# Optimization experiments

Hardware: AMD Instinct MI355X
Metric: run time of the kernel (lower is better)

Reference implementation:

```python
import jax, jax.numpy as jnp
import numpy as np

EPS = 1e-7  # K.epsilon()
SIZE_IN, IN_CAPS, KSIZE, STRIDE, CAPS, ROUTINGS = 14, 32, 3, 2, 32, 3
SIZE_OUT = (SIZE_IN - KSIZE) // STRIDE + 1  # 6
P = SIZE_OUT * SIZE_OUT          # 36 parent positions
C = KSIZE * KSIZE * IN_CAPS      # 288 child capsules per parent


def _child_parent_map():
    idx = []
    valid = range(0, SIZE_IN - KSIZE + 1, STRIDE)
    for row in valid:
        for col in valid:
            for kr in range(KSIZE):
                start = (row + kr) * SIZE_IN + col
                idx.extend(range(start, start + KSIZE))
    return np.asarray(idx, dtype=np.int32).reshape(P, KSIZE * KSIZE)

CPM = _child_parent_map()  # [P, K^2] static gather indices


def _em_routing(in_act, votes, beta_a, beta_v):
    # in_act: [B,P,C,1,1]; votes: [B,P,C,O,16]
    O = CAPS
    rr = jnp.full(votes.shape[:4] + (1,), 1.0 / O, dtype=votes.dtype)
    bv = beta_v.reshape(1, 1, 1, O, 1)
    ba = beta_a.reshape(1, 1, 1, O)
    out_act = means = None
    for i in range(ROUTINGS):
        lambd = 0.01 * (1.0 - 0.95 ** i)
        # ---- M step ----
        rr_scaled = rr * in_act                                   # [B,P,C,O,1]
        rr_sum = jnp.sum(rr_scaled, axis=2, keepdims=True)        # [B,P,1,O,1]
        means = jnp.sum(rr_scaled * votes, axis=2, keepdims=True) / (rr_sum + EPS)  # [B,P,1,O,16]
        std = jnp.sqrt(jnp.sum(rr_scaled * jnp.square(votes - means), axis=2, keepdims=True) / (rr_sum + EPS))
        costs = bv + jnp.log(std + EPS) * rr_sum                  # [B,P,1,O,16]
        out_act = jax.nn.sigmoid(lambd * (ba - jnp.sum(costs, axis=-1)))[..., None]  # [B,P,1,O,1]
        # ---- E step ----
        if i < ROUTINGS - 1:
            prob_exp = -jnp.sum(jnp.square(votes - means) / (2.0 * jnp.square(std) + EPS), axis=-1, keepdims=True)
            prob_main = -jnp.sum(jnp.log(std + EPS), axis=-1, keepdims=True)
            zz = jnp.log(out_act + EPS) + prob_main + prob_exp   # [B,P,C,O,1]
            rr = jax.nn.softmax(zz, axis=3)
    return out_act, means


def setup_inputs() -> dict:
    key = jax.random.key(0)
    k1, k2, k3, k4, k5 = jax.random.split(key, 5)
    B = 8
    return {
        "in_act": jax.random.uniform(k1, (B, SIZE_IN, SIZE_IN, IN_CAPS, 1), dtype=jnp.float32),
        "in_pose": jax.random.normal(k2, (B, SIZE_IN, SIZE_IN, IN_CAPS, 4, 4), dtype=jnp.float32),
        "W": jax.random.normal(k3, (1, 1, C, CAPS, 4, 4), dtype=jnp.float32) * 0.1,
        "beta_a": jax.random.normal(k4, (CAPS,), dtype=jnp.float32),
        "beta_v": jax.random.normal(k5, (CAPS,), dtype=jnp.float32),
    }


def reference(in_act, in_pose, W, beta_a, beta_v):
    B = in_act.shape[0]
    act = in_act.reshape(B, SIZE_IN * SIZE_IN, IN_CAPS)
    pose = in_pose.reshape(B, SIZE_IN * SIZE_IN, IN_CAPS, 4, 4)
    # gather children for each parent window -> [B,P,C,...]
    act_g = act[:, CPM].reshape(B, P, C, 1, 1)
    pose_g = pose[:, CPM].reshape(B, P, C, 4, 4)
    # votes[b,p,c,o,i,j] = sum_k pose_g[b,p,c,i,k] * W[c,o,k,j]
    votes = jnp.einsum('bpcik,cokj->bpcoij', pose_g, W.reshape(C, CAPS, 4, 4))
    votes = votes.reshape(B, P, C, CAPS, 16)
    out_act, out_pose = _em_routing(act_g, votes, beta_a, beta_v)
    out_act = out_act.reshape(B, SIZE_OUT, SIZE_OUT, CAPS, 1)
    out_pose = out_pose.reshape(B, SIZE_OUT, SIZE_OUT, CAPS, 4, 4)
    return out_act, out_pose
```

## Files before the change

kernel.cpp:

```cpp
#include <hip/hip_runtime.h>
#include <math.h>

#define EPS 1e-7f

constexpr int SIZE_IN = 14;
constexpr int P_  = 36;
constexpr int Cc  = 288;
constexpr int O_  = 32;
constexpr int THREADS = 256;

struct __align__(16) SMem {
    float pose[Cc * 16];
    float act[Cc];
    float red[4][O_][33];
    float mean[O_][17];
    float iv[O_][17];
    float zb[O_];
};

#define F4_TO_ARR(dst, off, f4) \
    dst[(off)+0] = (f4).x; dst[(off)+1] = (f4).y; dst[(off)+2] = (f4).z; dst[(off)+3] = (f4).w;

template<int CTRL>
__device__ __forceinline__ float dppf(float x) {
    int xi = __builtin_bit_cast(int, x);
    return __builtin_bit_cast(float,
        __builtin_amdgcn_update_dpp(xi, xi, CTRL, 0xf, 0xf, true));
}
__device__ __forceinline__ float swz16(float x) {
    return __builtin_bit_cast(float,
        __builtin_amdgcn_ds_swizzle(__builtin_bit_cast(int, x), 0x401F));
}
__device__ __forceinline__ float red32_max(float x) {
    x = fmaxf(x, dppf<0xB1>(x));
    x = fmaxf(x, dppf<0x4E>(x));
    x = fmaxf(x, dppf<0x141>(x));
    x = fmaxf(x, dppf<0x140>(x));
    x = fmaxf(x, swz16(x));
    return x;
}
__device__ __forceinline__ float red32_sum(float x) {
    x += dppf<0xB1>(x);
    x += dppf<0x4E>(x);
    x += dppf<0x141>(x);
    x += dppf<0x140>(x);
    x += swz16(x);
    return x;
}
__device__ __forceinline__ float red16_sum(float x) {
    x += dppf<0xB1>(x);
    x += dppf<0x4E>(x);
    x += dppf<0x141>(x);
    x += dppf<0x140>(x);
    return x;
}

template<bool HASE, bool LAST>
__device__ __forceinline__ void em_pass(
    SMem& sm, const float* __restrict__ W,
    const float* __restrict__ beta_a, const float* __restrict__ beta_v,
    float lambda, int bp, float* __restrict__ out)
{
    const int tid = threadIdx.x;
    const int o  = tid & 31;
    const int ci = tid >> 5;

    float m[16], iv[16], zb = 0.f;
    if (HASE) {
        #pragma unroll
        for (int j = 0; j < 16; ++j) { m[j] = sm.mean[o][j]; iv[j] = sm.iv[o][j]; }
        zb = sm.zb[o];
    }

    float S0 = 0.f, S1[16], S2[16];
    #pragma unroll
    for (int j = 0; j < 16; ++j) { S1[j] = 0.f; S2[j] = 0.f; }

    const float4* wp0 = reinterpret_cast<const float4*>(W + (size_t)(ci * O_ + o) * 16);
    float4 nw0 = wp0[0], nw1 = wp0[1], nw2 = wp0[2], nw3 = wp0[3];
    const float4* pp0 = reinterpret_cast<const float4*>(&sm.pose[ci * 16]);
    float4 np0 = pp0[0], np1 = pp0[1], np2 = pp0[2], np3 = pp0[3];

    #pragma unroll 2
    for (int t = 0; t < 36; ++t) {
        const int c = t * 8 + ci;
        float w[16], q[16];
        F4_TO_ARR(w, 0, nw0) F4_TO_ARR(w, 4, nw1) F4_TO_ARR(w, 8, nw2) F4_TO_ARR(w, 12, nw3)
        F4_TO_ARR(q, 0, np0) F4_TO_ARR(q, 4, np1) F4_TO_ARR(q, 8, np2) F4_TO_ARR(q, 12, np3)
        if (t + 1 < 36) {
            const int cn = c + 8;
            const float4* wn = reinterpret_cast<const float4*>(W + (size_t)(cn * O_ + o) * 16);
            nw0 = wn[0]; nw1 = wn[1]; nw2 = wn[2]; nw3 = wn[3];
            const float4* pn = reinterpret_cast<const float4*>(&sm.pose[cn * 16]);
            np0 = pn[0]; np1 = pn[1]; np2 = pn[2]; np3 = pn[3];
        }

        float v[16];
        #pragma unroll
        for (int i = 0; i < 4; ++i) {
            #pragma unroll
            for (int jj = 0; jj < 4; ++jj) {
                float acc = q[i*4+0] * w[0*4+jj];
                acc = fmaf(q[i*4+1], w[1*4+jj], acc);
                acc = fmaf(q[i*4+2], w[2*4+jj], acc);
                acc = fmaf(q[i*4+3], w[3*4+jj], acc);
                v[i*4+jj] = acc;
            }
        }

        float ws;
        if (HASE) {
            float s = 0.f;
            #pragma unroll
            for (int j = 0; j < 16; ++j) { float d = v[j] - m[j]; s = fmaf(d * d, iv[j], s); }
            float zz = zb - s;
            float mx = red32_max(zz);
            float e = __expf(zz - mx);
            float sum = red32_sum(e);
            float rr = e / sum;
            ws = rr * sm.act[c];
        } else {
            ws = sm.act[c] * (1.0f / 32.0f);
        }

        S0 += ws;
        #pragma unroll
        for (int j = 0; j < 16; ++j) {
            float t0 = ws * v[j];
            S1[j] += t0;
            S2[j] = fmaf(t0, v[j], S2[j]);
        }
    }

    S0 += __shfl_xor(S0, 32);
    #pragma unroll
    for (int j = 0; j < 16; ++j) {
        S1[j] += __shfl_xor(S1[j], 32);
        S2[j] += __shfl_xor(S2[j], 32);
    }
    if (!(tid & 32)) {
        const int wv = tid >> 6;
        float* r = sm.red[wv][o];
        r[0] = S0;
        #pragma unroll
        for (int j = 0; j < 16; ++j) { r[1 + j] = S1[j]; r[17 + j] = S2[j]; }
    }
    __syncthreads();

    #pragma unroll
    for (int half = 0; half < 2; ++half) {
        const int of = (tid >> 4) + half * 16, jf = tid & 15;
        const float* r0 = sm.red[0][of];
        const float* r1 = sm.red[1][of];
        const float* r2 = sm.red[2][of];
        const float* r3 = sm.red[3][of];
        float s0 = r0[0] + r1[0] + r2[0] + r3[0];
        float s1 = r0[1+jf] + r1[1+jf] + r2[1+jf] + r3[1+jf];
        float s2 = r0[17+jf] + r1[17+jf] + r2[17+jf] + r3[17+jf];
        float denom = s0 + EPS;
        float mj = s1 / denom;
        float varn = fmaxf(s2 - 2.f * mj * s1 + mj * mj * s0, 0.f);
        float sd = sqrtf(varn / denom);
        float sumlog = red16_sum(__logf(sd + EPS));
        if (!LAST) {
            sm.mean[of][jf] = mj;
            sm.iv[of][jf] = 1.f / fmaf(2.f * sd, sd, EPS);
            if (jf == 0) {
                float cost = fmaf(16.f, beta_v[of], s0 * sumlog);
                float oact = 1.f / (1.f + __expf(-(lambda * (beta_a[of] - cost))));
                sm.zb[of] = __logf(oact + EPS) - sumlog;
            }
        } else {
            out[8 * P_ * O_ + (size_t)(bp * O_ + of) * 16 + jf] = mj;
            if (jf == 0) {
                float cost = fmaf(16.f, beta_v[of], s0 * sumlog);
                float oact = 1.f / (1.f + __expf(-(lambda * (beta_a[of] - cost))));
                out[bp * O_ + of] = oact;
            }
        }
    }
    __syncthreads();
}

__global__ __launch_bounds__(THREADS, 2) void convcaps_kernel(
    const float* __restrict__ in_act, const float* __restrict__ in_pose,
    const float* __restrict__ W, const float* __restrict__ beta_a,
    const float* __restrict__ beta_v, float* __restrict__ out)
{
    __shared__ SMem sm;
    const int bp = blockIdx.x;
    const int b  = bp / P_;
    const int p  = bp % P_;
    const int tid = threadIdx.x;
    const int row0 = (p / 6) * 2, col0 = (p % 6) * 2;

    for (int f = tid; f < 9 * 128; f += THREADS) {
        const int qw = f >> 7, r = f & 127;
        const int pix = (row0 + qw / 3) * SIZE_IN + (col0 + qw % 3);
        reinterpret_cast<float4*>(sm.pose)[qw * 128 + r] =
            reinterpret_cast<const float4*>(in_pose + (size_t)(b * 196 + pix) * 512)[r];
    }
    for (int idx = tid; idx < Cc; idx += THREADS) {
        const int qw = idx >> 5, ic = idx & 31;
        const int pix = (row0 + qw / 3) * SIZE_IN + (col0 + qw % 3);
        sm.act[idx] = in_act[(size_t)(b * 196 + pix) * 32 + ic];
    }
    __syncthreads();

    em_pass<false, false>(sm, W, beta_a, beta_v, 0.0f,      bp, out);
    em_pass<true,  false>(sm, W, beta_a, beta_v, 0.0005f,   bp, out);
    em_pass<true,  true >(sm, W, beta_a, beta_v, 0.000975f, bp, out);
}

extern "C" void kernel_launch(void* const* d_in, const int* in_sizes, int n_in,
                              void* d_out, int out_size, void* d_ws, size_t ws_size,
                              hipStream_t stream) {
    const float* in_act  = (const float*)d_in[0];
    const float* in_pose = (const float*)d_in[1];
    const float* W       = (const float*)d_in[2];
    const float* beta_a  = (const float*)d_in[3];
    const float* beta_v  = (const float*)d_in[4];
    float* out = (float*)d_out;

    convcaps_kernel<<<dim3(8 * P_), dim3(THREADS), 0, stream>>>(
        in_act, in_pose, W, beta_a, beta_v, out);
}
```

Before: 143.8 us.

## Split child capsules across four blocks per parent with multi-kernel routing passes

Each routing iteration becomes its own kernel launch, and each parent position's 288 children are split across 4 blocks. Partial sufficient statistics go to a workspace buffer and are reduced by the next pass or by a final output kernel. The grid grows from 288 to 1152 blocks, which is meant to fill the GPU's compute units better. The cost is three extra launches, global round-trips for the partial sums, and pose/act reloaded in every pass. The old fused kernel is kept as a fallback when the workspace is too small.

```diff
diff --git a/kernel.cpp b/kernel.cpp
--- a/kernel.cpp
+++ b/kernel.cpp
@@ -7,7 +7,233 @@
 constexpr int P_  = 36;
 constexpr int Cc  = 288;
 constexpr int O_  = 32;
+constexpr int G_  = 4;
+constexpr int CG  = Cc / G_;
+constexpr int NTG = CG / 8;
 constexpr int THREADS = 256;
+constexpr int NBP = 8 * P_;
+
+template<int CTRL>
+__device__ __forceinline__ float dppf(float x) {
+    int xi = __builtin_bit_cast(int, x);
+    return __builtin_bit_cast(float,
+        __builtin_amdgcn_update_dpp(xi, xi, CTRL, 0xf, 0xf, true));
+}
+__device__ __forceinline__ float swz16(float x) {
+    return __builtin_bit_cast(float,
+        __builtin_amdgcn_ds_swizzle(__builtin_bit_cast(int, x), 0x401F));
+}
+__device__ __forceinline__ float red32_max(float x) {
+    x = fmaxf(x, dppf<0xB1>(x));
+    x = fmaxf(x, dppf<0x4E>(x));
+    x = fmaxf(x, dppf<0x141>(x));
+    x = fmaxf(x, dppf<0x140>(x));
+    x = fmaxf(x, swz16(x));
+    return x;
+}
+__device__ __forceinline__ float red32_sum(float x) {
+    x += dppf<0xB1>(x);
+    x += dppf<0x4E>(x);
+    x += dppf<0x141>(x);
+    x += dppf<0x140>(x);
+    x += swz16(x);
+    return x;
+}
+__device__ __forceinline__ float red16_sum(float x) {
+    x += dppf<0xB1>(x);
+    x += dppf<0x4E>(x);
+    x += dppf<0x141>(x);
+    x += dppf<0x140>(x);
+    return x;
+}
+
+#define F4_TO_ARR(dst, off, f4) \
+    dst[(off)+0] = (f4).x; dst[(off)+1] = (f4).y; dst[(off)+2] = (f4).z; dst[(off)+3] = (f4).w;
+
+struct __align__(16) PassMem {
+    float pose[CG * 16];
+    float act[CG];
+    float red[4][O_][33];
+    float mean[O_][17];
+    float iv[O_][17];
+    float zb[O_];
+};
+
+template<bool HASE>
+__global__ __launch_bounds__(THREADS, 2) void caps_pass(
+    const float* __restrict__ in_act, const float* __restrict__ in_pose,
+    const float* __restrict__ W, const float* __restrict__ beta_a,
+    const float* __restrict__ beta_v, const float* __restrict__ Pprev,
+    float* __restrict__ Pout, float lambda_prev)
+{
+    __shared__ PassMem sm;
+    const int blk = blockIdx.x;
+    const int bp = blk >> 2, g = blk & 3;
+    const int b  = bp / P_,  p = bp % P_;
+    const int tid = threadIdx.x;
+    const int row0 = (p / 6) * 2, col0 = (p % 6) * 2;
+
+    for (int f = tid; f < CG * 4; f += THREADS) {
+        const int fq = g * (CG * 4) + f;
+        const int qw = fq >> 7, r = fq & 127;
+        const int pix = (row0 + qw / 3) * SIZE_IN + (col0 + qw % 3);
+        reinterpret_cast<float4*>(sm.pose)[f] =
+            reinterpret_cast<const float4*>(in_pose + (size_t)(b * 196 + pix) * 512)[r];
+    }
+    for (int idx = tid; idx < CG; idx += THREADS) {
+        const int c = g * CG + idx;
+        const int qw = c >> 5, ic = c & 31;
+        const int pix = (row0 + qw / 3) * SIZE_IN + (col0 + qw % 3);
+        sm.act[idx] = in_act[(size_t)(b * 196 + pix) * 32 + ic];
+    }
+
+    if (HASE) {
+        const float* base = Pprev + (size_t)bp * G_ * O_ * 33;
+        #pragma unroll
+        for (int half = 0; half < 2; ++half) {
+            const int of = (tid >> 4) + half * 16, jf = tid & 15;
+            float s0 = 0.f, s1 = 0.f, s2 = 0.f;
+            #pragma unroll
+            for (int gg = 0; gg < G_; ++gg) {
+                const float* r = base + ((size_t)gg * O_ + of) * 33;
+                s0 += r[0]; s1 += r[1 + jf]; s2 += r[17 + jf];
+            }
+            float denom = s0 + EPS;
+            float mj = s1 / denom;
+            float varn = fmaxf(s2 - 2.f * mj * s1 + mj * mj * s0, 0.f);
+            float sd = sqrtf(varn / denom);
+            float sumlog = red16_sum(__logf(sd + EPS));
+            sm.mean[of][jf] = mj;
+            sm.iv[of][jf] = 1.f / fmaf(2.f * sd, sd, EPS);
+            if (jf == 0) {
+                float cost = fmaf(16.f, beta_v[of], s0 * sumlog);
+                float oact = 1.f / (1.f + __expf(-(lambda_prev * (beta_a[of] - cost))));
+                sm.zb[of] = __logf(oact + EPS) - sumlog;
+            }
+        }
+    }
+    __syncthreads();
+
+    const int o  = tid & 31;
+    const int ci = tid >> 5;
+
+    float m[16], iv[16], zb = 0.f;
+    if (HASE) {
+        #pragma unroll
+        for (int j = 0; j < 16; ++j) { m[j] = sm.mean[o][j]; iv[j] = sm.iv[o][j]; }
+        zb = sm.zb[o];
+    }
+
+    float S0 = 0.f, S1[16], S2[16];
+    #pragma unroll
+    for (int j = 0; j < 16; ++j) { S1[j] = 0.f; S2[j] = 0.f; }
+
+    const float4* wp0 = reinterpret_cast<const float4*>(W + (size_t)((g * CG + ci) * O_ + o) * 16);
+    float4 nw0 = wp0[0], nw1 = wp0[1], nw2 = wp0[2], nw3 = wp0[3];
+    const float4* pp0 = reinterpret_cast<const float4*>(&sm.pose[ci * 16]);
+    float4 np0 = pp0[0], np1 = pp0[1], np2 = pp0[2], np3 = pp0[3];
+
+    #pragma unroll 2
+    for (int t = 0; t < NTG; ++t) {
+        const int cl = t * 8 + ci;
+        float w[16], q[16];
+        F4_TO_ARR(w, 0, nw0) F4_TO_ARR(w, 4, nw1) F4_TO_ARR(w, 8, nw2) F4_TO_ARR(w, 12, nw3)
+        F4_TO_ARR(q, 0, np0) F4_TO_ARR(q, 4, np1) F4_TO_ARR(q, 8, np2) F4_TO_ARR(q, 12, np3)
+        if (t + 1 < NTG) {
+            const int cn = g * CG + cl + 8;
+            const float4* wn = reinterpret_cast<const float4*>(W + (size_t)(cn * O_ + o) * 16);
+            nw0 = wn[0]; nw1 = wn[1]; nw2 = wn[2]; nw3 = wn[3];
+            const float4* pn = reinterpret_cast<const float4*>(&sm.pose[(cl + 8) * 16]);
+            np0 = pn[0]; np1 = pn[1]; np2 = pn[2]; np3 = pn[3];
+        }
+
+        float v[16];
+        #pragma unroll
+        for (int i = 0; i < 4; ++i) {
+            #pragma unroll
+            for (int jj = 0; jj < 4; ++jj) {
+                float acc = q[i*4+0] * w[0*4+jj];
+                acc = fmaf(q[i*4+1], w[1*4+jj], acc);
+                acc = fmaf(q[i*4+2], w[2*4+jj], acc);
+                acc = fmaf(q[i*4+3], w[3*4+jj], acc);
+                v[i*4+jj] = acc;
+            }
+        }
+
+        float ws;
+        if (HASE) {
+            float s = 0.f;
+            #pragma unroll
+            for (int j = 0; j < 16; ++j) { float d = v[j] - m[j]; s = fmaf(d * d, iv[j], s); }
+            float zz = zb - s;
+            float mx = red32_max(zz);
+            float e = __expf(zz - mx);
+            float sum = red32_sum(e);
+            ws = (e / sum) * sm.act[cl];
+        } else {
+            ws = sm.act[cl] * (1.0f / 32.0f);
+        }
+
+        S0 += ws;
+        #pragma unroll
+        for (int j = 0; j < 16; ++j) {
+            float t0 = ws * v[j];
+            S1[j] += t0;
+            S2[j] = fmaf(t0, v[j], S2[j]);
+        }
+    }
+
+    S0 += __shfl_xor(S0, 32);
+    #pragma unroll
+    for (int j = 0; j < 16; ++j) {
+        S1[j] += __shfl_xor(S1[j], 32);
+        S2[j] += __shfl_xor(S2[j], 32);
+    }
+    if (!(tid & 32)) {
+        const int wv = tid >> 6;
+        float* r = sm.red[wv][o];
+        r[0] = S0;
+        #pragma unroll
+        for (int j = 0; j < 16; ++j) { r[1 + j] = S1[j]; r[17 + j] = S2[j]; }
+    }
+    __syncthreads();
+
+    float* slot = Pout + (size_t)(bp * G_ + g) * O_ * 33;
+    for (int idx = tid; idx < O_ * 33; idx += THREADS) {
+        const int oo = idx / 33, k = idx - oo * 33;
+        slot[idx] = sm.red[0][oo][k] + sm.red[1][oo][k] + sm.red[2][oo][k] + sm.red[3][oo][k];
+    }
+}
+
+__global__ __launch_bounds__(THREADS, 2) void caps_out(
+    const float* __restrict__ Pfin, const float* __restrict__ beta_a,
+    const float* __restrict__ beta_v, float* __restrict__ out, float lambda)
+{
+    const int bp = blockIdx.x;
+    const int tid = threadIdx.x;
+    const float* base = Pfin + (size_t)bp * G_ * O_ * 33;
+    #pragma unroll
+    for (int half = 0; half < 2; ++half) {
+        const int of = (tid >> 4) + half * 16, jf = tid & 15;
+        float s0 = 0.f, s1 = 0.f, s2 = 0.f;
+        #pragma unroll
+        for (int gg = 0; gg < G_; ++gg) {
+            const float* r = base + ((size_t)gg * O_ + of) * 33;
+            s0 += r[0]; s1 += r[1 + jf]; s2 += r[17 + jf];
+        }
+        float denom = s0 + EPS;
+        float mj = s1 / denom;
+        float varn = fmaxf(s2 - 2.f * mj * s1 + mj * mj * s0, 0.f);
+        float sd = sqrtf(varn / denom);
+        float sumlog = red16_sum(__logf(sd + EPS));
+        out[NBP * O_ + ((size_t)bp * O_ + of) * 16 + jf] = mj;
+        if (jf == 0) {
+            float cost = fmaf(16.f, beta_v[of], s0 * sumlog);
+            float oact = 1.f / (1.f + __expf(-(lambda * (beta_a[of] - cost))));
+            out[bp * O_ + of] = oact;
+        }
+    }
+}
 
 struct __align__(16) SMem {
     float pose[Cc * 16];
@@ -17,43 +243,6 @@
     float iv[O_][17];
     float zb[O_];
 };
-
-#define F4_TO_ARR(dst, off, f4) \
-    dst[(off)+0] = (f4).x; dst[(off)+1] = (f4).y; dst[(off)+2] = (f4).z; dst[(off)+3] = (f4).w;
-
-template<int CTRL>
-__device__ __forceinline__ float dppf(float x) {
-    int xi = __builtin_bit_cast(int, x);
-    return __builtin_bit_cast(float,
-        __builtin_amdgcn_update_dpp(xi, xi, CTRL, 0xf, 0xf, true));
-}
-__device__ __forceinline__ float swz16(float x) {
-    return __builtin_bit_cast(float,
-        __builtin_amdgcn_ds_swizzle(__builtin_bit_cast(int, x), 0x401F));
-}
-__device__ __forceinline__ float red32_max(float x) {
-    x = fmaxf(x, dppf<0xB1>(x));
-    x = fmaxf(x, dppf<0x4E>(x));
-    x = fmaxf(x, dppf<0x141>(x));
-    x = fmaxf(x, dppf<0x140>(x));
-    x = fmaxf(x, swz16(x));
-    return x;
-}
-__device__ __forceinline__ float red32_sum(float x) {
-    x += dppf<0xB1>(x);
-    x += dppf<0x4E>(x);
-    x += dppf<0x141>(x);
-    x += dppf<0x140>(x);
-    x += swz16(x);
-    return x;
-}
-__device__ __forceinline__ float red16_sum(float x) {
-    x += dppf<0xB1>(x);
-    x += dppf<0x4E>(x);
-    x += dppf<0x141>(x);
-    x += dppf<0x140>(x);
-    return x;
-}
 
 template<bool HASE, bool LAST>
 __device__ __forceinline__ void em_pass(
@@ -117,8 +306,7 @@
             float mx = red32_max(zz);
             float e = __expf(zz - mx);
             float sum = red32_sum(e);
-            float rr = e / sum;
-            ws = rr * sm.act[c];
+            ws = (e / sum) * sm.act[c];
         } else {
             ws = sm.act[c] * (1.0f / 32.0f);
         }
@@ -171,7 +359,7 @@
                 sm.zb[of] = __logf(oact + EPS) - sumlog;
             }
         } else {
-            out[8 * P_ * O_ + (size_t)(bp * O_ + of) * 16 + jf] = mj;
+            out[NBP * O_ + ((size_t)bp * O_ + of) * 16 + jf] = mj;
             if (jf == 0) {
                 float cost = fmaf(16.f, beta_v[of], s0 * sumlog);
                 float oact = 1.f / (1.f + __expf(-(lambda * (beta_a[of] - cost))));
@@ -182,7 +370,7 @@
     __syncthreads();
 }
 
-__global__ __launch_bounds__(THREADS, 2) void convcaps_kernel(
+__global__ __launch_bounds__(THREADS, 2) void convcaps_fused(
     const float* __restrict__ in_act, const float* __restrict__ in_pose,
     const float* __restrict__ W, const float* __restrict__ beta_a,
     const float* __restrict__ beta_v, float* __restrict__ out)
@@ -222,6 +410,22 @@
     const float* beta_v  = (const float*)d_in[4];
     float* out = (float*)d_out;
 
-    convcaps_kernel<<<dim3(8 * P_), dim3(THREADS), 0, stream>>>(
-        in_act, in_pose, W, beta_a, beta_v, out);
-}
+    const size_t buf_elems = (size_t)NBP * G_ * O_ * 33;
+    const size_t need = 2 * buf_elems * sizeof(float);
+
+    if (ws_size >= need) {
+        float* P1 = (float*)d_ws;
+        float* P2 = P1 + buf_elems;
+        dim3 gp(NBP * G_), blk(THREADS);
+        caps_pass<false><<<gp, blk, 0, stream>>>(in_act, in_pose, W, beta_a, beta_v,
+                                                 nullptr, P1, 0.0f);
+        caps_pass<true><<<gp, blk, 0, stream>>>(in_act, in_pose, W, beta_a, beta_v,
+                                                P1, P2, 0.0f);
+        caps_pass<true><<<gp, blk, 0, stream>>>(in_act, in_pose, W, beta_a, beta_v,
+                                                P2, P1, 0.0005f);
+        caps_out<<<dim3(NBP), blk, 0, stream>>>(P1, beta_a, beta_v, out, 0.000975f);
+    } else {
+        convcaps_fused<<<dim3(NBP), dim3(THREADS), 0, stream>>>(
+            in_act, in_pose, W, beta_a, beta_v, out);
+    }
+}
```

After: 240.6 us. +67.3%, slower.
